# Performance work log

Hardware: AMD Instinct MI355X
Metric: run time of the kernel (lower is better)

The kernel has to match this reference:

```python
import jax, jax.numpy as jnp
import numpy as np

# dims: 3 bert layers averaged, B batch, T_SUB subword tokens (excl. CLS), W words, D=768 bert dim
B, T_SUB, W, D = 64, 512, 256, 768
H = 20          # lstm_hidden
CAP_DIM = 10
CAP_TYPES = 4
IN_DIM = D + CAP_DIM


def setup_inputs() -> dict:
    key = jax.random.key(0)
    ks = jax.random.split(key, 10)
    hiddens = jax.random.normal(ks[0], (3, B, T_SUB + 1, D), jnp.float32)  # [CLS] at pos 0
    # nondecreasing word ids, each word gets exactly T_SUB//W subwords (all segments non-empty)
    bert2toks = jnp.tile(jnp.repeat(jnp.arange(W), T_SUB // W)[None, :], (B, 1)).astype(jnp.int32)
    cap_inds = jax.random.randint(ks[1], (B, W), 0, CAP_TYPES)
    cap_table = jax.random.normal(ks[2], (CAP_TYPES, CAP_DIM), jnp.float32) * 0.1
    s = 1.0 / np.sqrt(H)
    u = lambda k, shp: jax.random.uniform(k, shp, jnp.float32, -s, s)
    w_ih_f = u(ks[3], (4 * H, IN_DIM))
    w_hh_f = u(ks[4], (4 * H, H))
    b_f = u(ks[5], (4 * H,))  # b_ih + b_hh fused
    w_ih_b = u(ks[6], (4 * H, IN_DIM))
    w_hh_b = u(ks[7], (4 * H, H))
    b_b = u(ks[8], (4 * H,))
    return {"hiddens": hiddens, "bert2toks": bert2toks, "cap_inds": cap_inds,
            "cap_table": cap_table, "w_ih_f": w_ih_f, "w_hh_f": w_hh_f, "b_f": b_f,
            "w_ih_b": w_ih_b, "w_hh_b": w_hh_b, "b_b": b_b}


def _lstm_dir(xs, w_ih, w_hh, b, reverse):
    # xs: [B, W, IN_DIM] -> hs: [B, W, H]
    xs_t = jnp.swapaxes(xs, 0, 1)  # [W, B, IN]
    if reverse:
        xs_t = xs_t[::-1]
    h0 = jnp.zeros((xs.shape[0], H), xs.dtype)

    def step(carry, xt):
        h, c = carry
        g = xt @ w_ih.T + h @ w_hh.T + b  # [B, 4H], pytorch gate order i,f,g,o
        i, f, gg, o = jnp.split(g, 4, axis=-1)
        c = jax.nn.sigmoid(f) * c + jax.nn.sigmoid(i) * jnp.tanh(gg)
        h = jax.nn.sigmoid(o) * jnp.tanh(c)
        return (h, c), h

    _, hs = jax.lax.scan(step, (h0, h0), xs_t)
    if reverse:
        hs = hs[::-1]
    return jnp.swapaxes(hs, 0, 1)


def reference(hiddens, bert2toks, cap_inds, cap_table,
              w_ih_f, w_hh_f, b_f, w_ih_b, w_hh_b, b_b):
    # mean over the 3 selected bert layers
    means = jnp.mean(hiddens, axis=0)          # [B, T_SUB+1, D]
    sub = means[:, 1:T_SUB + 1]                # skip [CLS]: means[i+1] indexing
    # ragged subword->word mean pooling as a segment mean
    flat_ids = (bert2toks + jnp.arange(B, dtype=bert2toks.dtype)[:, None] * W).reshape(-1)
    sums = jax.ops.segment_sum(sub.reshape(B * T_SUB, D), flat_ids, num_segments=B * W)
    cnts = jax.ops.segment_sum(jnp.ones((B * T_SUB, 1), sub.dtype), flat_ids, num_segments=B * W)
    word_h = (sums / cnts).reshape(B, W, D)
    cap_emb = cap_table[cap_inds]              # [B, W, CAP_DIM]
    x = jnp.concatenate([word_h, cap_emb], axis=-1)  # [B, W, IN_DIM]
    out = jnp.concatenate([
        _lstm_dir(x, w_ih_f, w_hh_f, b_f, False),
        _lstm_dir(x, w_ih_b, w_hh_b, b_b, True),
    ], axis=-1)                                # [B, W, 2H]
    return out
```

## Files before the change

### kernel.cpp

```cpp
#include <hip/hip_runtime.h>
#include <math.h>

#define BB 64
#define T_SUB 512
#define WW 256
#define DD 768
#define HH 20
#define CAP_DIM 10
#define IN_DIM 778
#define KPAD 800
#define G4 80
#define NOUT 160
#define LOG2E 1.44269504f

typedef _Float16 f16x8 __attribute__((ext_vector_type(8)));
typedef float f32x4 __attribute__((ext_vector_type(4)));
typedef unsigned int uint2v __attribute__((ext_vector_type(2)));

#define WP_OFF   ((size_t)0)
#define SEG_OFF  ((size_t)256000)
#define X_OFF    ((size_t)387072)

__global__ __launch_bounds__(256) void k_prep(
    const float* __restrict__ wf, const float* __restrict__ wb,
    const int* __restrict__ b2t,
    _Float16* __restrict__ wp, int2* __restrict__ seg)
{
    int blk = blockIdx.x;
    if (blk < NOUT) {
        int j = blk;
        const float* src = (j < G4) ? (wf + (size_t)j * IN_DIM)
                                    : (wb + (size_t)(j - G4) * IN_DIM);
        for (int k = threadIdx.x; k < KPAD; k += 256)
            wp[(size_t)j * KPAD + k] = (k < IN_DIM) ? (_Float16)(LOG2E * src[k])
                                                    : (_Float16)0.f;
    } else {
        int b = blk - NOUT, w = threadIdx.x;
        const int* row = b2t + (size_t)b * T_SUB;
        int lo = 0, hi = T_SUB;
        while (lo < hi) { int m = (lo + hi) >> 1; if (row[m] < w) lo = m + 1; else hi = m; }
        int lo2 = lo, hi2 = T_SUB;
        while (lo2 < hi2) { int m = (lo2 + hi2) >> 1; if (row[m] < w + 1) lo2 = m + 1; else hi2 = m; }
        seg[(size_t)b * WW + w] = make_int2(lo, lo2 - lo);
    }
}

__global__ __launch_bounds__(256) void k_mean(
    const float* __restrict__ hiddens, const int2* __restrict__ seg,
    const int* __restrict__ cap_inds, const float* __restrict__ cap_table,
    _Float16* __restrict__ x)
{
    int idx = blockIdx.x * 256 + threadIdx.x;
    int d2 = idx % 50;
    int bw = idx / 50;
    int b = bw >> 8;
    int2 sg = seg[bw];
    int lo = sg.x, cnt = sg.y;
    const size_t LSTR = (size_t)BB * (T_SUB + 1) * DD;
    const float* rowp = hiddens + ((size_t)b * (T_SUB + 1) + lo + 1) * DD;
    float inv = 1.0f / (3.0f * (float)(cnt > 0 ? cnt : 1));
    bool bmean = (d2 + 50) < 96;
    f16x8 ra, rb;

    if (cnt == 2 && bmean) {
        const float* pa  = rowp + d2 * 8;
        const float* pb_ = rowp + (d2 + 50) * 8;
        float4 A0 = *(const float4*)(pa);                float4 A1 = *(const float4*)(pa + 4);
        float4 A2 = *(const float4*)(pa + DD);           float4 A3 = *(const float4*)(pa + DD + 4);
        float4 A4 = *(const float4*)(pa + LSTR);         float4 A5 = *(const float4*)(pa + LSTR + 4);
        float4 A6 = *(const float4*)(pa + LSTR + DD);    float4 A7 = *(const float4*)(pa + LSTR + DD + 4);
        float4 A8 = *(const float4*)(pa + 2*LSTR);       float4 A9 = *(const float4*)(pa + 2*LSTR + 4);
        float4 Aa = *(const float4*)(pa + 2*LSTR + DD);  float4 Ab = *(const float4*)(pa + 2*LSTR + DD + 4);
        float4 B0 = *(const float4*)(pb_);               float4 B1 = *(const float4*)(pb_ + 4);
        float4 B2 = *(const float4*)(pb_ + DD);          float4 B3 = *(const float4*)(pb_ + DD + 4);
        float4 B4 = *(const float4*)(pb_ + LSTR);        float4 B5 = *(const float4*)(pb_ + LSTR + 4);
        float4 B6 = *(const float4*)(pb_ + LSTR + DD);   float4 B7 = *(const float4*)(pb_ + LSTR + DD + 4);
        float4 B8 = *(const float4*)(pb_ + 2*LSTR);      float4 B9 = *(const float4*)(pb_ + 2*LSTR + 4);
        float4 Ba = *(const float4*)(pb_ + 2*LSTR + DD); float4 Bb = *(const float4*)(pb_ + 2*LSTR + DD + 4);
        ra[0] = (_Float16)((A0.x+A2.x+A4.x+A6.x+A8.x+Aa.x) * inv);
        ra[1] = (_Float16)((A0.y+A2.y+A4.y+A6.y+A8.y+Aa.y) * inv);
        ra[2] = (_Float16)((A0.z+A2.z+A4.z+A6.z+A8.z+Aa.z) * inv);
        ra[3] = (_Float16)((A0.w+A2.w+A4.w+A6.w+A8.w+Aa.w) * inv);
        ra[4] = (_Float16)((A1.x+A3.x+A5.x+A7.x+A9.x+Ab.x) * inv);
        ra[5] = (_Float16)((A1.y+A3.y+A5.y+A7.y+A9.y+Ab.y) * inv);
        ra[6] = (_Float16)((A1.z+A3.z+A5.z+A7.z+A9.z+Ab.z) * inv);
        ra[7] = (_Float16)((A1.w+A3.w+A5.w+A7.w+A9.w+Ab.w) * inv);
        rb[0] = (_Float16)((B0.x+B2.x+B4.x+B6.x+B8.x+Ba.x) * inv);
        rb[1] = (_Float16)((B0.y+B2.y+B4.y+B6.y+B8.y+Ba.y) * inv);
        rb[2] = (_Float16)((B0.z+B2.z+B4.z+B6.z+B8.z+Ba.z) * inv);
        rb[3] = (_Float16)((B0.w+B2.w+B4.w+B6.w+B8.w+Ba.w) * inv);
        rb[4] = (_Float16)((B1.x+B3.x+B5.x+B7.x+B9.x+Bb.x) * inv);
        rb[5] = (_Float16)((B1.y+B3.y+B5.y+B7.y+B9.y+Bb.y) * inv);
        rb[6] = (_Float16)((B1.z+B3.z+B5.z+B7.z+B9.z+Bb.z) * inv);
        rb[7] = (_Float16)((B1.w+B3.w+B5.w+B7.w+B9.w+Bb.w) * inv);
    } else {
        float a[8], bacc[8];
#pragma unroll
        for (int q = 0; q < 8; q++) { a[q] = 0.f; bacc[q] = 0.f; }
        for (int l = 0; l < 3; ++l)
            for (int ti = 0; ti < cnt; ++ti) {
                const float* p = rowp + l * LSTR + (size_t)ti * DD;
                float4 v0 = *(const float4*)(p + d2 * 8);
                float4 v1 = *(const float4*)(p + d2 * 8 + 4);
                a[0]+=v0.x; a[1]+=v0.y; a[2]+=v0.z; a[3]+=v0.w;
                a[4]+=v1.x; a[5]+=v1.y; a[6]+=v1.z; a[7]+=v1.w;
                if (bmean) {
                    float4 u0 = *(const float4*)(p + (d2 + 50) * 8);
                    float4 u1 = *(const float4*)(p + (d2 + 50) * 8 + 4);
                    bacc[0]+=u0.x; bacc[1]+=u0.y; bacc[2]+=u0.z; bacc[3]+=u0.w;
                    bacc[4]+=u1.x; bacc[5]+=u1.y; bacc[6]+=u1.z; bacc[7]+=u1.w;
                }
            }
#pragma unroll
        for (int q = 0; q < 8; q++) { ra[q] = (_Float16)(a[q] * inv); rb[q] = (_Float16)(bacc[q] * inv); }
    }
    if (!bmean) {
        int ci = cap_inds[bw];
#pragma unroll
        for (int q = 0; q < 8; q++) {
            int c = (d2 + 50 - 96) * 8 + q;
            rb[q] = (c < CAP_DIM) ? (_Float16)cap_table[ci * CAP_DIM + c] : (_Float16)0.f;
        }
    }
    *(f16x8*)(x + (size_t)bw * KPAD + d2 * 8) = ra;
    *(f16x8*)(x + (size_t)bw * KPAD + (d2 + 50) * 8) = rb;
}

__device__ __forceinline__ float xchg32(float v) {
    unsigned int a = __float_as_uint(v);
    uint2v r = __builtin_amdgcn_permlane32_swap(a, a, false, false);
    return __uint_as_float(r[0] ^ r[1] ^ a);
}
__device__ __forceinline__ float fex2(float v) { return __builtin_amdgcn_exp2f(v); }
__device__ __forceinline__ float frcp(float v) { return __builtin_amdgcn_rcpf(v); }

__global__ __launch_bounds__(320) void k_lstm(
    const _Float16* __restrict__ x, const _Float16* __restrict__ wp,
    const float* __restrict__ bias_f, const float* __restrict__ bias_b,
    const float* __restrict__ whh_f, const float* __restrict__ whh_b,
    float* __restrict__ out)
{
    __shared__ _Float16 gb[WW * G4];
    int dir  = blockIdx.x >> 6;
    int b    = blockIdx.x & 63;
    int t    = threadIdx.x;
    int wv   = t >> 6;
    int lane = t & 63;

    if (wv >= 1) {
        int col  = lane & 15;
        int koff = (lane >> 4) * 8;
        int wbase = (wv - 1) * 64;
        const _Float16* bp = wp + (size_t)(dir * G4 + col) * KPAD + koff;
        float bias_v[5];
#pragma unroll
        for (int nf = 0; nf < 5; nf++)
            bias_v[nf] = LOG2E * (dir ? bias_b : bias_f)[nf * 16 + col];
        f32x4 acc[4][5];
#pragma unroll
        for (int mt = 0; mt < 4; mt++)
#pragma unroll
            for (int nf = 0; nf < 5; nf++)
#pragma unroll
                for (int r = 0; r < 4; r++) acc[mt][nf][r] = 0.f;
        for (int k0 = 0; k0 < KPAD; k0 += 32) {
            f16x8 bf[5];
#pragma unroll
            for (int nf = 0; nf < 5; nf++)
                bf[nf] = *(const f16x8*)(bp + (size_t)nf * 16 * KPAD + k0);
#pragma unroll
            for (int mt = 0; mt < 4; mt++) {
                int arow = b * 256 + wbase + mt * 16 + (lane & 15);
                f16x8 af = *(const f16x8*)(x + (size_t)arow * KPAD + koff + k0);
#pragma unroll
                for (int nf = 0; nf < 5; nf++)
                    acc[mt][nf] = __builtin_amdgcn_mfma_f32_16x16x32_f16(af, bf[nf], acc[mt][nf], 0, 0, 0);
            }
        }
#pragma unroll
        for (int mt = 0; mt < 4; mt++)
#pragma unroll
            for (int nf = 0; nf < 5; nf++) {
                int g = nf * 16 + col;
                int pcol = (g % 40) * 2 + (g / 40);
#pragma unroll
                for (int r = 0; r < 4; r++) {
                    int word = wbase + mt * 16 + (lane >> 4) * 4 + r;
                    gb[word * G4 + pcol] = (_Float16)(acc[mt][nf][r] + bias_v[nf]);
                }
            }
        __syncthreads();
        return;
    }

    const float* whh = dir ? whh_b : whh_f;
    int j = lane & 31; if (j > 19) j = 19;
    bool low = lane < 32;
    float mm = low ? 1.f : 2.f;
    float aa = low ? 0.f : -1.f;
    int coff = low ? (40 + 2 * j) : (2 * j);
    float w0[HH], w1[HH];
    {
        int r0 = low ? (20 + j) : j;
        int r1 = low ? (60 + j) : (40 + j);
#pragma unroll
        for (int k = 0; k < HH; k++) {
            w0[k] = LOG2E * whh[r0 * HH + k];
            w1[k] = LOG2E * whh[r1 * HH + k];
        }
    }
    __syncthreads();

    __builtin_amdgcn_s_setprio(1);
    const float TCM = -2.f * LOG2E;
    float h = 0.f, c = 0.f;
    int w = dir ? (WW - 1) : 0;
    int stepd = dir ? -1 : 1;

    union { unsigned int u; _Float16 hx[2]; } cu;
    cu.u = *(const unsigned int*)(gb + w * G4 + coff);
    float2 pre = make_float2((float)cu.hx[0], (float)cu.hx[1]);

    for (int sl = 0; sl < WW; ++sl) {
        int wn = w + stepd;
        int wnc = wn < 0 ? 0 : (wn > 255 ? 255 : wn);
        union { unsigned int u; _Float16 hx[2]; } nu;
        nu.u = *(const unsigned int*)(gb + wnc * G4 + coff);
        float a0a = pre.x, a0b = 0.f, a1a = pre.y, a1b = 0.f;
#pragma unroll
        for (int k = 0; k < 10; k++) {
            float hk  = __uint_as_float(__builtin_amdgcn_readlane(__float_as_uint(h), k));
            float hk2 = __uint_as_float(__builtin_amdgcn_readlane(__float_as_uint(h), k + 10));
            a0a = fmaf(hk,  w0[k],      a0a);
            a1a = fmaf(hk,  w1[k],      a1a);
            a0b = fmaf(hk2, w0[k + 10], a0b);
            a1b = fmaf(hk2, w1[k + 10], a1b);
        }
        float a0 = a0a + a0b, a1 = a1a + a1b;
        float u0 = frcp(1.f + fex2(-a0));
        float uu = frcp(1.f + fex2(-mm * a1));
        float u1 = fmaf(uu, mm, aa);
        float p  = u0 * u1;
        float ps = xchg32(p);
        c = fmaf(u0, c, ps);
        float tc = fmaf(2.f, frcp(1.f + fex2(TCM * c)), -1.f);
        h = u1 * tc;
        if (lane < HH)
            out[((size_t)b * WW + w) * (2 * HH) + dir * HH + lane] = h;
        pre = make_float2((float)nu.hx[0], (float)nu.hx[1]);
        w = wn;
    }
    __builtin_amdgcn_s_setprio(0);
}

extern "C" void kernel_launch(void* const* d_in, const int* in_sizes, int n_in,
                              void* d_out, int out_size, void* d_ws, size_t ws_size,
                              hipStream_t stream) {
    const float* hiddens   = (const float*)d_in[0];
    const int*   bert2toks = (const int*)d_in[1];
    const int*   cap_inds  = (const int*)d_in[2];
    const float* cap_table = (const float*)d_in[3];
    const float* w_ih_f    = (const float*)d_in[4];
    const float* w_hh_f    = (const float*)d_in[5];
    const float* b_f       = (const float*)d_in[6];
    const float* w_ih_b    = (const float*)d_in[7];
    const float* w_hh_b    = (const float*)d_in[8];
    const float* b_b       = (const float*)d_in[9];
    float* out = (float*)d_out;

    _Float16* wpad = (_Float16*)((char*)d_ws + WP_OFF);
    int2*     seg  = (int2*)((char*)d_ws + SEG_OFF);
    _Float16* x    = (_Float16*)((char*)d_ws + X_OFF);

    k_prep<<<NOUT + BB, 256, 0, stream>>>(w_ih_f, w_ih_b, bert2toks, wpad, seg);
    k_mean<<<(BB * WW * 50) / 256, 256, 0, stream>>>(hiddens, seg, cap_inds, cap_table, x);
    k_lstm<<<128, 320, 0, stream>>>(x, wpad, b_f, b_b, w_hh_f, w_hh_b, out);
}
```

Before: 135.8 us.

## Fuse segment search into mean kernel, use nontemporal loads, widen LSTM recurrence ILP

Moves the per-word binary search of subword segments out of the prep kernel and into the mean kernel, so each block computes the few segments it needs in shared memory. This removes the seg round trip through global memory. The hidden-state reads become nontemporal loads to avoid cache pollution on a large streaming input. The recurrent dot product in the LSTM step is split into four independent accumulator chains to shorten its serial dependency. In exchange, the mean kernel adds a block-wide sync and some redundant binary searches per block.

Measured after the change: 171.5 us. +26.3%, slower.

```diff
diff --git a/kernel.cpp b/kernel.cpp
--- a/kernel.cpp
+++ b/kernel.cpp
@@ -18,43 +18,49 @@
 typedef unsigned int uint2v __attribute__((ext_vector_type(2)));
 
 #define WP_OFF   ((size_t)0)
-#define SEG_OFF  ((size_t)256000)
 #define X_OFF    ((size_t)387072)
 
 __global__ __launch_bounds__(256) void k_prep(
     const float* __restrict__ wf, const float* __restrict__ wb,
-    const int* __restrict__ b2t,
-    _Float16* __restrict__ wp, int2* __restrict__ seg)
+    _Float16* __restrict__ wp)
 {
-    int blk = blockIdx.x;
-    if (blk < NOUT) {
-        int j = blk;
-        const float* src = (j < G4) ? (wf + (size_t)j * IN_DIM)
-                                    : (wb + (size_t)(j - G4) * IN_DIM);
-        for (int k = threadIdx.x; k < KPAD; k += 256)
-            wp[(size_t)j * KPAD + k] = (k < IN_DIM) ? (_Float16)(LOG2E * src[k])
-                                                    : (_Float16)0.f;
-    } else {
-        int b = blk - NOUT, w = threadIdx.x;
-        const int* row = b2t + (size_t)b * T_SUB;
-        int lo = 0, hi = T_SUB;
-        while (lo < hi) { int m = (lo + hi) >> 1; if (row[m] < w) lo = m + 1; else hi = m; }
-        int lo2 = lo, hi2 = T_SUB;
-        while (lo2 < hi2) { int m = (lo2 + hi2) >> 1; if (row[m] < w + 1) lo2 = m + 1; else hi2 = m; }
-        seg[(size_t)b * WW + w] = make_int2(lo, lo2 - lo);
-    }
+    int j = blockIdx.x;
+    const float* src = (j < G4) ? (wf + (size_t)j * IN_DIM)
+                                : (wb + (size_t)(j - G4) * IN_DIM);
+    for (int k = threadIdx.x; k < KPAD; k += 256)
+        wp[(size_t)j * KPAD + k] = (k < IN_DIM) ? (_Float16)(LOG2E * src[k])
+                                                : (_Float16)0.f;
+}
+
+__device__ __forceinline__ f32x4 ntl(const float* p) {
+    return __builtin_nontemporal_load((const f32x4*)p);
 }
 
 __global__ __launch_bounds__(256) void k_mean(
-    const float* __restrict__ hiddens, const int2* __restrict__ seg,
+    const float* __restrict__ hiddens, const int* __restrict__ b2t,
     const int* __restrict__ cap_inds, const float* __restrict__ cap_table,
     _Float16* __restrict__ x)
 {
+    __shared__ int2 segs[8];
+    int wb0 = (blockIdx.x * 256) / 50;
+    int nw  = (blockIdx.x * 256 + 255) / 50 - wb0 + 1;
+    if (threadIdx.x < nw) {
+        int bw_ = wb0 + threadIdx.x;
+        int b_ = bw_ >> 8, w_ = bw_ & 255;
+        const int* row = b2t + (size_t)b_ * T_SUB;
+        int lo = 0, hi = T_SUB;
+        while (lo < hi) { int m = (lo + hi) >> 1; if (row[m] < w_) lo = m + 1; else hi = m; }
+        int lo2 = lo, hi2 = T_SUB;
+        while (lo2 < hi2) { int m = (lo2 + hi2) >> 1; if (row[m] < w_ + 1) lo2 = m + 1; else hi2 = m; }
+        segs[threadIdx.x] = make_int2(lo, lo2 - lo);
+    }
+    __syncthreads();
+
     int idx = blockIdx.x * 256 + threadIdx.x;
     int d2 = idx % 50;
     int bw = idx / 50;
     int b = bw >> 8;
-    int2 sg = seg[bw];
+    int2 sg = segs[bw - wb0];
     int lo = sg.x, cnt = sg.y;
     const size_t LSTR = (size_t)BB * (T_SUB + 1) * DD;
     const float* rowp = hiddens + ((size_t)b * (T_SUB + 1) + lo + 1) * DD;
@@ -65,34 +71,21 @@
     if (cnt == 2 && bmean) {
         const float* pa  = rowp + d2 * 8;
         const float* pb_ = rowp + (d2 + 50) * 8;
-        float4 A0 = *(const float4*)(pa);                float4 A1 = *(const float4*)(pa + 4);
-        float4 A2 = *(const float4*)(pa + DD);           float4 A3 = *(const float4*)(pa + DD + 4);
-        float4 A4 = *(const float4*)(pa + LSTR);         float4 A5 = *(const float4*)(pa + LSTR + 4);
-        float4 A6 = *(const float4*)(pa + LSTR + DD);    float4 A7 = *(const float4*)(pa + LSTR + DD + 4);
-        float4 A8 = *(const float4*)(pa + 2*LSTR);       float4 A9 = *(const float4*)(pa + 2*LSTR + 4);
-        float4 Aa = *(const float4*)(pa + 2*LSTR + DD);  float4 Ab = *(const float4*)(pa + 2*LSTR + DD + 4);
-        float4 B0 = *(const float4*)(pb_);               float4 B1 = *(const float4*)(pb_ + 4);
-        float4 B2 = *(const float4*)(pb_ + DD);          float4 B3 = *(const float4*)(pb_ + DD + 4);
-        float4 B4 = *(const float4*)(pb_ + LSTR);        float4 B5 = *(const float4*)(pb_ + LSTR + 4);
-        float4 B6 = *(const float4*)(pb_ + LSTR + DD);   float4 B7 = *(const float4*)(pb_ + LSTR + DD + 4);
-        float4 B8 = *(const float4*)(pb_ + 2*LSTR);      float4 B9 = *(const float4*)(pb_ + 2*LSTR + 4);
-        float4 Ba = *(const float4*)(pb_ + 2*LSTR + DD); float4 Bb = *(const float4*)(pb_ + 2*LSTR + DD + 4);
-        ra[0] = (_Float16)((A0.x+A2.x+A4.x+A6.x+A8.x+Aa.x) * inv);
-        ra[1] = (_Float16)((A0.y+A2.y+A4.y+A6.y+A8.y+Aa.y) * inv);
-        ra[2] = (_Float16)((A0.z+A2.z+A4.z+A6.z+A8.z+Aa.z) * inv);
-        ra[3] = (_Float16)((A0.w+A2.w+A4.w+A6.w+A8.w+Aa.w) * inv);
-        ra[4] = (_Float16)((A1.x+A3.x+A5.x+A7.x+A9.x+Ab.x) * inv);
-        ra[5] = (_Float16)((A1.y+A3.y+A5.y+A7.y+A9.y+Ab.y) * inv);
-        ra[6] = (_Float16)((A1.z+A3.z+A5.z+A7.z+A9.z+Ab.z) * inv);
-        ra[7] = (_Float16)((A1.w+A3.w+A5.w+A7.w+A9.w+Ab.w) * inv);
-        rb[0] = (_Float16)((B0.x+B2.x+B4.x+B6.x+B8.x+Ba.x) * inv);
-        rb[1] = (_Float16)((B0.y+B2.y+B4.y+B6.y+B8.y+Ba.y) * inv);
-        rb[2] = (_Float16)((B0.z+B2.z+B4.z+B6.z+B8.z+Ba.z) * inv);
-        rb[3] = (_Float16)((B0.w+B2.w+B4.w+B6.w+B8.w+Ba.w) * inv);
-        rb[4] = (_Float16)((B1.x+B3.x+B5.x+B7.x+B9.x+Bb.x) * inv);
-        rb[5] = (_Float16)((B1.y+B3.y+B5.y+B7.y+B9.y+Bb.y) * inv);
-        rb[6] = (_Float16)((B1.z+B3.z+B5.z+B7.z+B9.z+Bb.z) * inv);
-        rb[7] = (_Float16)((B1.w+B3.w+B5.w+B7.w+B9.w+Bb.w) * inv);
+        f32x4 A[12], B[12];
+#pragma unroll
+        for (int l = 0; l < 3; ++l) {
+            A[l*4+0] = ntl(pa + l*LSTR);        A[l*4+1] = ntl(pa + l*LSTR + 4);
+            A[l*4+2] = ntl(pa + l*LSTR + DD);   A[l*4+3] = ntl(pa + l*LSTR + DD + 4);
+            B[l*4+0] = ntl(pb_ + l*LSTR);       B[l*4+1] = ntl(pb_ + l*LSTR + 4);
+            B[l*4+2] = ntl(pb_ + l*LSTR + DD);  B[l*4+3] = ntl(pb_ + l*LSTR + DD + 4);
+        }
+#pragma unroll
+        for (int q = 0; q < 4; q++) {
+            ra[q]     = (_Float16)((A[0][q]+A[2][q]+A[4][q]+A[6][q]+A[8][q]+A[10][q]) * inv);
+            ra[q + 4] = (_Float16)((A[1][q]+A[3][q]+A[5][q]+A[7][q]+A[9][q]+A[11][q]) * inv);
+            rb[q]     = (_Float16)((B[0][q]+B[2][q]+B[4][q]+B[6][q]+B[8][q]+B[10][q]) * inv);
+            rb[q + 4] = (_Float16)((B[1][q]+B[3][q]+B[5][q]+B[7][q]+B[9][q]+B[11][q]) * inv);
+        }
     } else {
         float a[8], bacc[8];
 #pragma unroll
@@ -100,15 +93,15 @@
         for (int l = 0; l < 3; ++l)
             for (int ti = 0; ti < cnt; ++ti) {
                 const float* p = rowp + l * LSTR + (size_t)ti * DD;
-                float4 v0 = *(const float4*)(p + d2 * 8);
-                float4 v1 = *(const float4*)(p + d2 * 8 + 4);
-                a[0]+=v0.x; a[1]+=v0.y; a[2]+=v0.z; a[3]+=v0.w;
-                a[4]+=v1.x; a[5]+=v1.y; a[6]+=v1.z; a[7]+=v1.w;
+                f32x4 v0 = ntl(p + d2 * 8);
+                f32x4 v1 = ntl(p + d2 * 8 + 4);
+#pragma unroll
+                for (int q = 0; q < 4; q++) { a[q] += v0[q]; a[q+4] += v1[q]; }
                 if (bmean) {
-                    float4 u0 = *(const float4*)(p + (d2 + 50) * 8);
-                    float4 u1 = *(const float4*)(p + (d2 + 50) * 8 + 4);
-                    bacc[0]+=u0.x; bacc[1]+=u0.y; bacc[2]+=u0.z; bacc[3]+=u0.w;
-                    bacc[4]+=u1.x; bacc[5]+=u1.y; bacc[6]+=u1.z; bacc[7]+=u1.w;
+                    f32x4 u0 = ntl(p + (d2 + 50) * 8);
+                    f32x4 u1 = ntl(p + (d2 + 50) * 8 + 4);
+#pragma unroll
+                    for (int q = 0; q < 4; q++) { bacc[q] += u0[q]; bacc[q+4] += u1[q]; }
                 }
             }
 #pragma unroll
@@ -133,6 +126,9 @@
 }
 __device__ __forceinline__ float fex2(float v) { return __builtin_amdgcn_exp2f(v); }
 __device__ __forceinline__ float frcp(float v) { return __builtin_amdgcn_rcpf(v); }
+__device__ __forceinline__ float rl(float v, int k) {
+    return __uint_as_float(__builtin_amdgcn_readlane(__float_as_uint(v), k));
+}
 
 __global__ __launch_bounds__(320) void k_lstm(
     const _Float16* __restrict__ x, const _Float16* __restrict__ wp,
@@ -226,17 +222,18 @@
         int wnc = wn < 0 ? 0 : (wn > 255 ? 255 : wn);
         union { unsigned int u; _Float16 hx[2]; } nu;
         nu.u = *(const unsigned int*)(gb + wnc * G4 + coff);
-        float a0a = pre.x, a0b = 0.f, a1a = pre.y, a1b = 0.f;
-#pragma unroll
-        for (int k = 0; k < 10; k++) {
-            float hk  = __uint_as_float(__builtin_amdgcn_readlane(__float_as_uint(h), k));
-            float hk2 = __uint_as_float(__builtin_amdgcn_readlane(__float_as_uint(h), k + 10));
-            a0a = fmaf(hk,  w0[k],      a0a);
-            a1a = fmaf(hk,  w1[k],      a1a);
-            a0b = fmaf(hk2, w0[k + 10], a0b);
-            a1b = fmaf(hk2, w1[k + 10], a1b);
-        }
-        float a0 = a0a + a0b, a1 = a1a + a1b;
+        float s0 = pre.x, s1 = 0.f, s2 = 0.f, s3 = 0.f;
+        float t0 = pre.y, t1 = 0.f, t2 = 0.f, t3 = 0.f;
+#pragma unroll
+        for (int k = 0; k < 5; k++) {
+            float h0 = rl(h, k), h1 = rl(h, k + 5), h2 = rl(h, k + 10), h3 = rl(h, k + 15);
+            s0 = fmaf(h0, w0[k],      s0);  s1 = fmaf(h1, w0[k + 5],  s1);
+            s2 = fmaf(h2, w0[k + 10], s2);  s3 = fmaf(h3, w0[k + 15], s3);
+            t0 = fmaf(h0, w1[k],      t0);  t1 = fmaf(h1, w1[k + 5],  t1);
+            t2 = fmaf(h2, w1[k + 10], t2);  t3 = fmaf(h3, w1[k + 15], t3);
+        }
+        float a0 = (s0 + s1) + (s2 + s3);
+        float a1 = (t0 + t1) + (t2 + t3);
         float u0 = frcp(1.f + fex2(-a0));
         float uu = frcp(1.f + fex2(-mm * a1));
         float u1 = fmaf(uu, mm, aa);
@@ -269,10 +266,9 @@
     float* out = (float*)d_out;
 
     _Float16* wpad = (_Float16*)((char*)d_ws + WP_OFF);
-    int2*     seg  = (int2*)((char*)d_ws + SEG_OFF);
     _Float16* x    = (_Float16*)((char*)d_ws + X_OFF);
 
-    k_prep<<<NOUT + BB, 256, 0, stream>>>(w_ih_f, w_ih_b, bert2toks, wpad, seg);
-    k_mean<<<(BB * WW * 50) / 256, 256, 0, stream>>>(hiddens, seg, cap_inds, cap_table, x);
+    k_prep<<<NOUT, 256, 0, stream>>>(w_ih_f, w_ih_b, wpad);
+    k_mean<<<(BB * WW * 50) / 256, 256, 0, stream>>>(hiddens, bert2toks, cap_inds, cap_table, x);
     k_lstm<<<128, 320, 0, stream>>>(x, wpad, b_f, b_b, w_hh_f, w_hh_b, out);
 }
```
